# Kernel tuning notes

Measured on AMD Instinct MI355X. Metric: run time of the kernel, lower is better.

The kernel has to match this reference:

```python
import jax, jax.numpy as jnp
import numpy as np

B, H, W = 4, 192, 192
CIN, CB, CM = 64, 16, 256   # backbone out, bottleneck, mask channels
TOPK = 16
TEMP = 1.0
COLOR_NORM = 1.0
BN_EPS = 1e-5


def setup_inputs() -> dict:
    key = jax.random.key(0)
    k0, k1, k2, k3 = jax.random.split(key, 4)
    img = jax.random.uniform(k0, (B, 3, H, W), jnp.float32)
    base_feat = jax.random.normal(k1, (B, CIN, H, W), jnp.float32)
    w_bneck = jax.random.normal(k2, (CB, CIN), jnp.float32) * 0.05
    b_bneck = jnp.zeros((CB,), jnp.float32)
    bn_gamma = jnp.ones((CB,), jnp.float32)
    bn_beta = jnp.zeros((CB,), jnp.float32)
    w_mask = jax.random.normal(k3, (CM, CB), jnp.float32) * 0.05
    return dict(img=img, base_feat=base_feat, w_bneck=w_bneck, b_bneck=b_bneck,
                bn_gamma=bn_gamma, bn_beta=bn_beta, w_mask=w_mask, num_colors=256)


def reference(img, base_feat, w_bneck, b_bneck, bn_gamma, bn_beta, w_mask, num_colors):
    b, _, h, w = img.shape
    # bottleneck: 1x1 conv + BatchNorm (training batch stats) + ReLU
    x = jnp.einsum('bchw,oc->bohw', base_feat, w_bneck) + b_bneck[None, :, None, None]
    mean = x.mean(axis=(0, 2, 3))
    var = x.var(axis=(0, 2, 3))
    x = (x - mean[None, :, None, None]) * jax.lax.rsqrt(var + BN_EPS)[None, :, None, None]
    feat = jax.nn.relu(x * bn_gamma[None, :, None, None] + bn_beta[None, :, None, None])
    # color mask: 1x1 conv (no bias) -> [B, 256, H, W]
    m = jnp.einsum('bchw,oc->bohw', feat, w_mask)
    # fold 256 channels into num_colors groups and sum -> [B, K, H, W]
    m = m.reshape(b, -1, num_colors, h, w).sum(axis=1)
    k = min(TOPK, num_colors)
    # top-k over the color axis, softmax, scatter back into sparse mask
    mt = jnp.transpose(m, (0, 2, 3, 1))              # [B, H, W, K]
    vals, idx = jax.lax.top_k(mt, k)                 # [B, H, W, k]
    sm = jax.nn.softmax(vals / TEMP, axis=-1)
    m_sp = jnp.zeros_like(mt).at[
        jnp.arange(b)[:, None, None, None],
        jnp.arange(h)[None, :, None, None],
        jnp.arange(w)[None, None, :, None],
        idx].set(sm)
    m_sp = jnp.transpose(m_sp, (0, 3, 1, 2))         # [B, K, H, W]
    # weighted color palette: avoid the [B,3,K,H,W] intermediate via einsum
    num = jnp.einsum('bchw,bkhw->bck', img, m_sp)    # [B, 3, K]
    den = m_sp.sum(axis=(2, 3))[:, None, :] + 1e-8   # [B, 1, K]
    color_palette = num / den / COLOR_NORM           # [B, 3, K]
    transformed_img = jnp.einsum('bkhw,bck->bchw', m_sp, color_palette)
    return transformed_img, m_sp, color_palette[:, :, :, None, None]
```

## Files before the change

kernel.cpp:

```cpp
#include <hip/hip_runtime.h>

#define HW    36864
#define NB    4
#define NCH   256
#define CIN   64
#define CB    16
#define NPIX  (NB*HW)
#define DELTA 1e-4f

typedef short bf16x8 __attribute__((ext_vector_type(8)));
typedef float f32x4  __attribute__((ext_vector_type(4)));

struct FlagEntry {
  unsigned pix;
  unsigned char cnt, need, r0, r1;
  unsigned char ks[8];
};


__device__ __forceinline__ unsigned short bf16_rne(float x) {
  unsigned u = __float_as_uint(x);
  unsigned r = u + 0x7fffu + ((u >> 16) & 1u);
  return (unsigned short)(r >> 16);
}
__device__ __forceinline__ float bf16_tof(unsigned short h) {
  return __uint_as_float(((unsigned)h) << 16);
}


template<bool ASC>
__device__ __forceinline__ void bitonic16(float* v) {
  #pragma unroll
  for (int K = 2; K <= 16; K <<= 1) {
    #pragma unroll
    for (int J = K >> 1; J > 0; J >>= 1) {
      #pragma unroll
      for (int i = 0; i < 16; ++i) {
        int l = i ^ J;
        if (l > i) {
          bool up = (((i & K) == 0) == ASC);
          float a = v[i], b = v[l];
          float lo = fminf(a, b), hi = fmaxf(a, b);
          v[i] = up ? lo : hi;
          v[l] = up ? hi : lo;
        }
      }
    }
  }
}

__device__ __forceinline__ void bmerge16_desc(float* v) {
  #pragma unroll
  for (int J = 8; J > 0; J >>= 1) {
    #pragma unroll
    for (int i = 0; i < 16; ++i) {
      int l = i ^ J;
      if (l > i) {
        float a = v[i], b = v[l];
        float lo = fminf(a, b), hi = fmaxf(a, b);
        v[i] = hi; v[l] = lo;
      }
    }
  }
}


__global__ void k0_zero(unsigned* flagcnt) { *flagcnt = 0u; }


__global__ __launch_bounds__(256) void k1_conv(
    const float* __restrict__ bfeat, const float* __restrict__ wb,
    const float* __restrict__ bb, float* __restrict__ xout,
    double* __restrict__ part)
{
  __shared__ float wbT[CIN][CB];
  __shared__ double redS[4][CB];
  __shared__ double redQ[4][CB];
  const int t = threadIdx.x;
  for (int i = t; i < CIN*CB; i += 256) {
    int o = i >> 6, c = i & 63;
    wbT[c][o] = wb[i];
  }
  __syncthreads();

  const int blk = blockIdx.x;
  const int b = blk / 144, seg = blk % 144;
  const int p = seg * 256 + t;
  const float* bfb = bfeat + (size_t)b * CIN * HW;

  float acc[CB];
  #pragma unroll
  for (int o = 0; o < CB; ++o) acc[o] = bb[o];

  for (int c = 0; c < CIN; ++c) {
    float v = bfb[(size_t)c*HW + p];
    #pragma unroll
    for (int o4 = 0; o4 < 4; ++o4) {
      float4 w4 = *(const float4*)&wbT[c][o4*4];
      acc[o4*4+0] = fmaf(v, w4.x, acc[o4*4+0]);
      acc[o4*4+1] = fmaf(v, w4.y, acc[o4*4+1]);
      acc[o4*4+2] = fmaf(v, w4.z, acc[o4*4+2]);
      acc[o4*4+3] = fmaf(v, w4.w, acc[o4*4+3]);
    }
  }

  float* xb = xout + (size_t)b * CB * HW;
  #pragma unroll
  for (int o = 0; o < CB; ++o) xb[(size_t)o*HW + p] = acc[o];

  const int wv = t >> 6, lane = t & 63;
  #pragma unroll
  for (int o = 0; o < CB; ++o) {
    double a = (double)acc[o], q = a*a;
    for (int off = 32; off; off >>= 1) { a += __shfl_xor(a, off); q += __shfl_xor(q, off); }
    if (lane == 0) { redS[wv][o] = a; redQ[wv][o] = q; }
  }
  __syncthreads();
  if (t < CB) {
    double a = redS[0][t] + redS[1][t] + redS[2][t] + redS[3][t];
    part[(size_t)blk*32 + t] = a;
  } else if (t < 32) {
    int o = t - CB;
    double q = redQ[0][o] + redQ[1][o] + redQ[2][o] + redQ[3][o];
    part[(size_t)blk*32 + t] = q;
  }
}


__global__ __launch_bounds__(64) void k1b_stats(
    const double* __restrict__ part, const float* __restrict__ gam,
    const float* __restrict__ bet, double* __restrict__ st64, float* __restrict__ st32)
{
  __shared__ double sh[32];
  const int t = threadIdx.x;
  if (t < 32) {
    double a = 0.0;
    #pragma unroll 8
    for (int i = 0; i < 576; ++i) a += part[(size_t)i*32 + t];
    sh[t] = a;
  }
  __syncthreads();
  if (t < CB) {
    const double N = (double)NPIX;
    double mean = sh[t] / N;
    double var  = sh[16+t] / N - mean*mean;
    double rstd = 1.0 / sqrt(var + 1e-5);
    double scl = (double)gam[t] * rstd;
    double sft = (double)bet[t] - mean*scl;
    st64[t] = scl; st64[CB+t] = sft;
    st32[t] = (float)scl; st32[CB+t] = (float)sft;
  }
}


__global__ __launch_bounds__(256) void k1c_bfrag(
    const float* __restrict__ wm, short* __restrict__ bfrag)
{
  const int t = threadIdx.x;
  for (int e = t; e < 2048; e += 256) {
    const int v = e >> 10, ct = (e >> 6) & 15, l = e & 63;
    const int n = l & 15, g = l >> 4;
    const int col = ct*16 + n;
    short out[8];
    #pragma unroll
    for (int j = 0; j < 8; ++j) {
      const int k = g*8 + j;
      const int kk = k & 15;
      const bool hi_half = (k < 16);
      float w = wm[col*CB + kk];
      unsigned short hb = bf16_rne(w);
      float res = w - bf16_tof(hb);
      unsigned short lb = bf16_rne(res);
      bool use_hi = ((v == 0) == hi_half);
      out[j] = (short)(use_hi ? hb : lb);
    }
    bf16x8 pk;
    #pragma unroll
    for (int j = 0; j < 8; ++j) pk[j] = out[j];
    *(bf16x8*)&bfrag[(size_t)e * 8] = pk;
  }
}


__device__ __forceinline__ void k2_epilogue(int b, int p, int pxl,
    int selN, int nearN, int nselN,
    float* lcw, unsigned char* lidx, unsigned char* lnear,
    unsigned* cidx, float* cw, unsigned* flagcnt, FlagEntry* entries)
{
  int start = selN < 16 ? selN : 16;
  for (int j = start; j < 16; ++j) { lcw[pxl*16 + j] = 0.f; lidx[pxl*16 + j] = 0; }
  unsigned g = (unsigned)(b*HW + p);
  uint4 iv = *(uint4*)&lidx[pxl*16];
  ((uint4*)cidx)[g] = iv;
  float4* cwq = (float4*)cw;
  #pragma unroll
  for (int q = 0; q < 4; ++q) cwq[(size_t)g*4 + q] = *(float4*)&lcw[pxl*16 + q*4];
  bool flag = (nearN > 1) || (selN != 16);
  if (flag) {
    unsigned slot = atomicAdd(flagcnt, 1u);
    FlagEntry e;
    e.pix = g;
    int cnt = nearN < 8 ? nearN : 8;
    e.cnt = (unsigned char)cnt;
    int nsure = selN - nselN;
    int need = 16 - nsure;
    if (need < 0) need = 0;
    if (need > cnt) need = cnt;
    e.need = (unsigned char)need;
    e.r0 = (nearN > 8 || selN != 16) ? 1 : 0;
    e.r1 = 0;
    #pragma unroll
    for (int j = 0; j < 8; ++j) e.ks[j] = (j < cnt) ? lnear[pxl*8 + j] : 0;
    entries[slot] = e;
  }
}

#define MSTRIDE 260
#define PXB 32

__global__ __launch_bounds__(256, 4) void k2_main(
    const float* __restrict__ x, const short* __restrict__ bfrag,
    const float* __restrict__ st32, float* __restrict__ msp,
    unsigned* __restrict__ cidx, float* __restrict__ cw,
    unsigned* __restrict__ flagcnt, FlagEntry* __restrict__ entries)
{
  extern __shared__ char smem[];
  float* m_lds = (float*)smem;
  char* uni = smem + PXB*MSTRIDE*4;
  float* lcw = (float*)uni;
  unsigned char* lidx  = (unsigned char*)(uni + 2048);
  unsigned char* lnear = (unsigned char*)(uni + 2560);
  short* A_st = (short*)uni;

  const int t = threadIdx.x;
  const int blk = blockIdx.x;
  const int b = blk / 1152;
  const int p0 = (blk % 1152) * PXB;
  const float* xb = x + (size_t)b*CB*HW + p0;

  #pragma unroll
  for (int r = 0; r < 2; ++r) {
    int e = r*256 + t;
    int o = e >> 5, pl = e & 31;
    float vx = xb[(size_t)o*HW + pl];
    float f = fmaxf(0.f, fmaf(vx, st32[o], st32[CB+o]));
    unsigned short hb = bf16_rne(f);
    float res = f - bf16_tof(hb);
    unsigned short lb = bf16_rne(res);
    A_st[pl*40 + o]      = (short)hb;
    A_st[pl*40 + 16 + o] = (short)lb;
  }
  __syncthreads();

  const int w = t >> 6, l = t & 63;

  {
    const int rt = w & 1, ch = w >> 1;
    const int prow = rt*16 + (l & 15);
    const int k0 = (l >> 4) * 8;
    bf16x8 a = *(const bf16x8*)&A_st[prow*40 + k0];
    const int rowo = rt*16 + (l >> 4)*4;
    const int coln = l & 15;
    #pragma unroll
    for (int cc = 0; cc < 8; ++cc) {
      const int ct = ch*8 + cc;
      bf16x8 b1 = *(const bf16x8*)&bfrag[(size_t)(ct*64 + l)*8];
      bf16x8 b2 = *(const bf16x8*)&bfrag[(size_t)((16 + ct)*64 + l)*8];
      f32x4 acc = {0.f, 0.f, 0.f, 0.f};
      acc = __builtin_amdgcn_mfma_f32_16x16x32_bf16(a, b1, acc, 0, 0, 0);
      acc = __builtin_amdgcn_mfma_f32_16x16x32_bf16(a, b2, acc, 0, 0, 0);
      #pragma unroll
      for (int i = 0; i < 4; ++i)
        m_lds[(rowo + i)*MSTRIDE + ct*16 + coln] = acc[i];
    }
  }
  __syncthreads();

  const int p = t >> 3, q = t & 7;
  float mv[32];
  #pragma unroll
  for (int r = 0; r < 8; ++r) {
    const int c = (r + q) & 7;
    f32x4 v4 = *(const f32x4*)&m_lds[p*MSTRIDE + q*32 + c*4];
    mv[c*4+0] = v4[0]; mv[c*4+1] = v4[1]; mv[c*4+2] = v4[2]; mv[c*4+3] = v4[3];
  }

  float T[16], tmp[16];
  #pragma unroll
  for (int i = 0; i < 16; ++i) tmp[i] = mv[i];
  bitonic16<false>(tmp);
  #pragma unroll
  for (int i = 0; i < 16; ++i) T[i] = tmp[i];
  #pragma unroll
  for (int i = 0; i < 16; ++i) tmp[i] = mv[16 + i];
  bitonic16<true>(tmp);
  #pragma unroll
  for (int i = 0; i < 16; ++i) T[i] = fmaxf(T[i], tmp[i]);
  bmerge16_desc(T);
  #pragma unroll
  for (int mk = 1; mk <= 4; mk <<= 1) {
    float R[16];
    #pragma unroll
    for (int i = 0; i < 16; ++i) R[i] = fmaxf(T[i], __shfl_xor(T[15-i], mk));
    bmerge16_desc(R);
    #pragma unroll
    for (int i = 0; i < 16; ++i) T[i] = R[i];
  }
  const float tau = T[15], top = T[0];
  float Z = 0.f;
  #pragma unroll
  for (int i = 0; i < 16; ++i) Z += __expf(T[i] - top);
  const float iZ = 1.f / Z;

  int cs = 0, cn = 0, cns = 0;
  #pragma unroll
  for (int j = 0; j < 32; ++j) {
    float v = mv[j];
    bool s = (v >= tau);
    bool nr = (fabsf(v - tau) <= DELTA);
    cs += s ? 1 : 0; cn += nr ? 1 : 0; cns += (s && nr) ? 1 : 0;
  }
  const int lb_ = l & ~7;
  int offs = 0, offn = 0, selN = 0, nearN = 0, nselN = 0;
  #pragma unroll
  for (int j2 = 0; j2 < 8; ++j2) {
    int cv = __shfl(cs, lb_ + j2);
    int nv = __shfl(cn, lb_ + j2);
    int sv = __shfl(cns, lb_ + j2);
    selN += cv; nearN += nv; nselN += sv;
    if (j2 < q) { offs += cv; offn += nv; }
  }

  float* mspb = msp + (size_t)b*NCH*HW + p0;
  int isel = 0, inear = 0;
  #pragma unroll
  for (int j = 0; j < 32; ++j) {
    const int k = q*32 + j;
    float v = mv[j];
    bool s = (v >= tau);
    bool nr = (fabsf(v - tau) <= DELTA);
    float wv = s ? __expf(v - top) * iZ : 0.f;
    mspb[(size_t)k*HW + p] = wv;
    if (s) {
      int slot = offs + isel;
      if (slot < 16) { lcw[p*16 + slot] = wv; lidx[p*16 + slot] = (unsigned char)k; }
      ++isel;
    }
    if (nr) {
      int gs = offn + inear;
      if (gs < 8) lnear[p*8 + gs] = (unsigned char)k;
      ++inear;
    }
  }

  if (q == 0)
    k2_epilogue(b, p0 + p, p, selN, nearN, nselN, lcw, lidx, lnear,
                cidx, cw, flagcnt, entries);
}


__global__ __launch_bounds__(64) void k2b_fix(
    const float* __restrict__ bfeat, const float* __restrict__ wb,
    const float* __restrict__ bb, const float* __restrict__ wmg,
    const double* __restrict__ st64,
    const unsigned* __restrict__ flagcnt, const FlagEntry* __restrict__ entries,
    float* __restrict__ msp, unsigned* __restrict__ cidx, float* __restrict__ cw)
{
  __shared__ float wbT[CB][CIN];
  __shared__ float  wOrigL[16];
  __shared__ int    kOrigL[16];
  __shared__ float  wnL[8];
  __shared__ int    kL[8];
  __shared__ double tvL[16];
  __shared__ int    tiL[16];
  __shared__ float  wvL[16];

  const int lane = threadIdx.x;
  for (int i = lane; i < CB*CIN; i += 64) wbT[i >> 6][i & 63] = wb[i];
  __syncthreads();

  const unsigned n = *flagcnt;
  for (unsigned idx = blockIdx.x; idx < n; idx += gridDim.x) {
    FlagEntry e = entries[idx];
    const int b = (int)(e.pix / HW), p = (int)(e.pix % HW);

    const double v = (double)bfeat[(size_t)b*CIN*HW + (size_t)lane*HW + p];
    double ft[CB];
    #pragma unroll
    for (int o = 0; o < CB; ++o) {
      double s = v * (double)wbT[o][lane];
      #pragma unroll
      for (int off = 32; off; off >>= 1) s += __shfl_xor(s, off);
      s += (double)bb[o];
      ft[o] = fmax(0.0, s*st64[o] + st64[CB+o]);
    }

    float* mb = msp + (size_t)b*NCH*HW;
    unsigned char* cb_ = (unsigned char*)cidx + (size_t)e.pix*16;
    float* cwp = cw + (size_t)e.pix*16;

    if (e.r0) {
      double mm[4]; int kk4[4];
      #pragma unroll
      for (int u = 0; u < 4; ++u) {
        const int k = lane + 64*u; kk4[u] = k;
        const float* wr = wmg + k*CB;
        double a = 0.0;
        #pragma unroll
        for (int c = 0; c < CB; ++c) a = fma(ft[c], (double)wr[c], a);
        mm[u] = a;
      }
      for (int j = 0; j < 16; ++j) {
        double bm = mm[0]; int bk = kk4[0];
        #pragma unroll
        for (int u = 1; u < 4; ++u) {
          bool gt = (mm[u] > bm) || (mm[u] == bm && kk4[u] < bk);
          if (gt) { bm = mm[u]; bk = kk4[u]; }
        }
        #pragma unroll
        for (int off = 32; off; off >>= 1) {
          double om = __shfl_xor(bm, off);
          int ok = __shfl_xor(bk, off);
          bool gt = (om > bm) || (om == bm && ok < bk);
          if (gt) { bm = om; bk = ok; }
        }
        if (lane == 0) { tvL[j] = bm; tiL[j] = bk; }
        #pragma unroll
        for (int u = 0; u < 4; ++u) if (kk4[u] == bk) mm[u] = -1.0e300;
      }
      __syncthreads();
      const double top = tvL[0];
      double ej = (lane < 16) ? exp(tvL[lane] - top) : 0.0;
      double Z = ej;
      #pragma unroll
      for (int off = 32; off; off >>= 1) Z += __shfl_xor(Z, off);
      if (lane < 16) wvL[lane] = (float)(ej / Z);
      __syncthreads();
      int tiR[16]; float wvR[16];
      #pragma unroll
      for (int j = 0; j < 16; ++j) { tiR[j] = tiL[j]; wvR[j] = wvL[j]; }
      #pragma unroll
      for (int u = 0; u < 4; ++u) {
        const int k = lane + 64*u;
        float wv = 0.f;
        #pragma unroll
        for (int j = 0; j < 16; ++j) if (tiR[j] == k) wv = wvR[j];
        mb[(size_t)k*HW + p] = wv;
      }
      if (lane == 0) {
        unsigned used = 0; int on = 0;
        for (int it = 0; it < 16; ++it) {
          int bk = 1 << 20;
          #pragma unroll
          for (int j = 0; j < 16; ++j)
            if (!((used >> j) & 1u) && tiR[j] < bk) bk = tiR[j];
          if (bk >= (1 << 20)) break;
          float bw = 0.f;
          #pragma unroll
          for (int j = 0; j < 16; ++j)
            if (tiR[j] == bk) { bw = wvR[j]; used |= (1u << j); }
          if (bw != 0.f && on < 16) { cb_[on] = (unsigned char)bk; cwp[on] = bw; ++on; }
        }
        for (int j = on; j < 16; ++j) { cb_[j] = 0; cwp[j] = 0.f; }
      }
      __syncthreads();
      continue;
    }

    const int cnt = (e.cnt > 8) ? 8 : (int)e.cnt;
    int need = (int)e.need; if (need > cnt) need = cnt;

    if (lane < 16) { wOrigL[lane] = cwp[lane]; kOrigL[lane] = (int)cb_[lane]; }
    __syncthreads();

    const int myk = (lane < cnt) ? (int)e.ks[lane] : 0x7fffffff;
    double mj = 0.0;
    if (lane < cnt) {
      const float* wr = wmg + myk*CB;
      #pragma unroll
      for (int c = 0; c < CB; ++c) mj = fma(ft[c], (double)wr[c], mj);
    }
    float woldj = 0.f;
    if (lane < cnt) {
      #pragma unroll
      for (int q = 0; q < 16; ++q) {
        if (kOrigL[q] == myk && wOrigL[q] > 0.f) woldj = wOrigL[q];
      }
    }
    int rankj = 0;
    #pragma unroll
    for (int j2 = 0; j2 < 8; ++j2) {
      double m2 = __shfl(mj, j2);
      int k2v = __shfl(myk, j2);
      if (lane < cnt && j2 < cnt && j2 != lane) {
        bool gt = (m2 > mj) || (m2 == mj && k2v < myk);
        rankj += gt ? 1 : 0;
      }
    }
    float w2[8];
    #pragma unroll
    for (int j2 = 0; j2 < 8; ++j2) w2[j2] = __shfl(woldj, j2);
    int nw = 0;
    #pragma unroll
    for (int j2 = 0; j2 < 8; ++j2) if (j2 < cnt && w2[j2] > 0.f) ++nw;
    float wnj = 0.f;
    if (lane < cnt && rankj < need && rankj < nw) {
      #pragma unroll
      for (int cand = 0; cand < 8; ++cand) {
        if (cand < cnt && w2[cand] > 0.f) {
          float xv = w2[cand];
          int cgt = 0, cge = 0;
          #pragma unroll
          for (int j2 = 0; j2 < 8; ++j2)
            if (j2 < cnt && w2[j2] > 0.f) { cgt += (w2[j2] > xv); cge += (w2[j2] >= xv); }
          if (cgt <= rankj && rankj < cge) wnj = xv;
        }
      }
    }
    if (lane < cnt) mb[(size_t)myk*HW + p] = wnj;
    if (lane < 8)  { wnL[lane] = wnj; kL[lane] = myk; }
    __syncthreads();

    if (lane == 0) {
      int on = 0, ii = 0, jj = 0;
      while (ii < 16 || jj < cnt) {
        if (ii < 16 && wOrigL[ii] <= 0.f) { ++ii; continue; }
        int ko = (ii < 16) ? kOrigL[ii] : (1 << 20);
        int kj = (jj < cnt) ? kL[jj] : (1 << 20);
        if (ko >= (1 << 20) && kj >= (1 << 20)) break;
        if (ko < kj) {
          if (on < 16) { cb_[on] = (unsigned char)ko; cwp[on] = wOrigL[ii]; ++on; }
          ++ii;
        } else if (kj < ko) {
          if (wnL[jj] > 0.f && on < 16) { cb_[on] = (unsigned char)kj; cwp[on] = wnL[jj]; ++on; }
          ++jj;
        } else {
          if (wnL[jj] > 0.f && on < 16) { cb_[on] = (unsigned char)kj; cwp[on] = wnL[jj]; ++on; }
          ++ii; ++jj;
        }
      }
      for (int j = on; j < 16; ++j) { cb_[j] = 0; cwp[j] = 0.f; }
    }
    __syncthreads();
  }
}


__global__ __launch_bounds__(256) void k3_accum(
    const uint4* __restrict__ cidx, const float4* __restrict__ cw4,
    const float* __restrict__ img, float* __restrict__ part)
{
  __shared__ float acc[1024];
  const int t = threadIdx.x, blk = blockIdx.x;
  for (int i = t; i < 1024; i += 256) acc[i] = 0.f;
  __syncthreads();
  const int b = blk / 144;
  const int p = (blk % 144) * 256 + t;
  const float* imb = img + (size_t)b*3*HW;
  const int g = b*HW + p;
  uint4 iv = cidx[g];
  unsigned ivq[4] = {iv.x, iv.y, iv.z, iv.w};
  float r = imb[p], g_ = imb[HW + p], bl = imb[2*HW + p];
  #pragma unroll
  for (int q = 0; q < 4; ++q) {
    float4 wv = cw4[(size_t)g*4 + q];
    float wvv[4] = {wv.x, wv.y, wv.z, wv.w};
    #pragma unroll
    for (int u = 0; u < 4; ++u) {
      int k = (int)((ivq[q] >> (8*u)) & 255u);
      float wgt = wvv[u];
      atomicAdd(&acc[k],       wgt * r);
      atomicAdd(&acc[256 + k], wgt * g_);
      atomicAdd(&acc[512 + k], wgt * bl);
      atomicAdd(&acc[768 + k], wgt);
    }
  }
  __syncthreads();
  for (int i = t; i < 1024; i += 256) part[(size_t)blk*1024 + i] = acc[i];
}


__global__ __launch_bounds__(256) void k4_pal(
    const float* __restrict__ part, float* __restrict__ out_pal)
{
  __shared__ float acc[1024];
  const int b = blockIdx.x, t = threadIdx.x;
  for (int s = t; s < 1024; s += 256) {
    float a = 0.f;
    for (int i = 0; i < 144; ++i) a += part[(size_t)(b*144 + i)*1024 + s];
    acc[s] = a;
  }
  __syncthreads();
  for (int s = t; s < 768; s += 256) {
    int k = s & 255;
    float den = acc[768 + k] + 1e-8f;
    out_pal[(size_t)b*768 + s] = acc[s] / den;
  }
}


__global__ __launch_bounds__(256) void k5_img(
    const uint4* __restrict__ cidx, const float4* __restrict__ cw4,
    const float* __restrict__ pal, float* __restrict__ outimg)
{
  __shared__ float lp[768];
  const int t = threadIdx.x, blk = blockIdx.x;
  const int b = blk / 144;
  for (int i = t; i < 768; i += 256) lp[i] = pal[(size_t)b*768 + i];
  __syncthreads();
  const int p = (blk % 144) * 256 + t;
  const int g = b*HW + p;
  uint4 iv = cidx[g];
  unsigned ivq[4] = {iv.x, iv.y, iv.z, iv.w};
  float r = 0.f, g_ = 0.f, bl = 0.f;
  #pragma unroll
  for (int q = 0; q < 4; ++q) {
    float4 wv = cw4[(size_t)g*4 + q];
    float wvv[4] = {wv.x, wv.y, wv.z, wv.w};
    #pragma unroll
    for (int u = 0; u < 4; ++u) {
      int k = (int)((ivq[q] >> (8*u)) & 255u);
      float wgt = wvv[u];
      r  = fmaf(wgt, lp[k],       r);
      g_ = fmaf(wgt, lp[256 + k], g_);
      bl = fmaf(wgt, lp[512 + k], bl);
    }
  }
  float* ob = outimg + (size_t)b*3*HW;
  ob[p] = r; ob[HW + p] = g_; ob[2*HW + p] = bl;
}


extern "C" void kernel_launch(void* const* d_in, const int* in_sizes, int n_in,
                              void* d_out, int out_size, void* d_ws, size_t ws_size,
                              hipStream_t stream)
{
  const float* img   = (const float*)d_in[0];
  const float* bfeat = (const float*)d_in[1];
  const float* wb    = (const float*)d_in[2];
  const float* bb    = (const float*)d_in[3];
  const float* gam   = (const float*)d_in[4];
  const float* bet   = (const float*)d_in[5];
  const float* wm    = (const float*)d_in[6];

  float* out_img = (float*)d_out;
  float* out_msp = (float*)d_out + 442368;
  float* out_pal = (float*)d_out + 38191104;

  char* w = (char*)d_ws;
  float*     ws_x       = (float*)(w);
  double*    ws_part    = (double*)(w + 9437184);
  double*    ws_st64    = (double*)(w + 9584640);
  float*     ws_st32    = (float*)(w + 9584896);
  unsigned*  ws_flagcnt = (unsigned*)(w + 9585152);
  FlagEntry* ws_entries = (FlagEntry*)(w + 9585408);
  unsigned*  ws_cidx    = (unsigned*)(w + 11944704);
  float*     ws_cw      = (float*)(w + 14304000);
  float*     ws_nd      = ws_x;
  short*     ws_bfrag   = (short*)(w + 23741184);

  k0_zero<<<dim3(1), dim3(1), 0, stream>>>(ws_flagcnt);
  k1_conv<<<dim3(576), dim3(256), 0, stream>>>(bfeat, wb, bb, ws_x, ws_part);
  k1b_stats<<<dim3(1), dim3(64), 0, stream>>>(ws_part, gam, bet, ws_st64, ws_st32);
  k1c_bfrag<<<dim3(1), dim3(256), 0, stream>>>(wm, ws_bfrag);
  k2_main<<<dim3(4608), dim3(256), 36096, stream>>>(ws_x, ws_bfrag, ws_st32, out_msp,
                                                    ws_cidx, ws_cw, ws_flagcnt, ws_entries);
  k2b_fix<<<dim3(4096), dim3(64), 0, stream>>>(bfeat, wb, bb, wm, ws_st64,
                                               ws_flagcnt, ws_entries, out_msp, ws_cidx, ws_cw);
  k3_accum<<<dim3(576), dim3(256), 0, stream>>>((const uint4*)ws_cidx, (const float4*)ws_cw,
                                                img, ws_nd);
  k4_pal<<<dim3(4), dim3(256), 0, stream>>>(ws_nd, out_pal);
  k5_img<<<dim3(576), dim3(256), 0, stream>>>((const uint4*)ws_cidx, (const float4*)ws_cw,
                                              out_pal, out_img);
}
```

Before: 314.2 us.

## Split fused MFMA+top-k kernel into separate matmul and per-pixel selection kernels

The fused k2_main kernel is split in two. k2a_mfma computes the 256-channel mask via MFMA and writes raw logits to the output buffer. k2s_sel then rereads them with one thread per pixel, runs a streaming bitonic top-16, and rewrites the sparse softmax weights. This removes the cross-lane shuffle merges and the 8-lanes-per-pixel layout, but adds a full extra read and write of the roughly 150 MB mask tensor through global memory.

```diff
diff --git a/kernel.cpp b/kernel.cpp
--- a/kernel.cpp
+++ b/kernel.cpp
@@ -178,6 +178,73 @@
     #pragma unroll
     for (int j = 0; j < 8; ++j) pk[j] = out[j];
     *(bf16x8*)&bfrag[(size_t)e * 8] = pk;
+  }
+}
+
+
+#define MSTRIDE 261
+#define PXB 32
+
+__global__ __launch_bounds__(256, 4) void k2a_mfma(
+    const float* __restrict__ x, const short* __restrict__ bfrag,
+    const float* __restrict__ st32, float* __restrict__ msp)
+{
+  extern __shared__ char smem[];
+  float* m_lds = (float*)smem;
+  short* A_st = (short*)(smem + PXB*MSTRIDE*4);
+
+  const int t = threadIdx.x;
+  const int blk = blockIdx.x;
+  const int b = blk / 1152;
+  const int p0 = (blk % 1152) * PXB;
+  const float* xb = x + (size_t)b*CB*HW + p0;
+
+  #pragma unroll
+  for (int r = 0; r < 2; ++r) {
+    int e = r*256 + t;
+    int o = e >> 5, pl = e & 31;
+    float vx = xb[(size_t)o*HW + pl];
+    float f = fmaxf(0.f, fmaf(vx, st32[o], st32[CB+o]));
+    unsigned short hb = bf16_rne(f);
+    float res = f - bf16_tof(hb);
+    unsigned short lb = bf16_rne(res);
+    A_st[pl*40 + o]      = (short)hb;
+    A_st[pl*40 + 16 + o] = (short)lb;
+  }
+  __syncthreads();
+
+  const int w = t >> 6, l = t & 63;
+
+  {
+    const int rt = w & 1, ch = w >> 1;
+    const int prow = rt*16 + (l & 15);
+    const int k0 = (l >> 4) * 8;
+    bf16x8 a = *(const bf16x8*)&A_st[prow*40 + k0];
+    const int rowo = rt*16 + (l >> 4)*4;
+    const int coln = l & 15;
+    #pragma unroll
+    for (int cc = 0; cc < 8; ++cc) {
+      const int ct = ch*8 + cc;
+      bf16x8 b1 = *(const bf16x8*)&bfrag[(size_t)(ct*64 + l)*8];
+      bf16x8 b2 = *(const bf16x8*)&bfrag[(size_t)((16 + ct)*64 + l)*8];
+      f32x4 acc = {0.f, 0.f, 0.f, 0.f};
+      acc = __builtin_amdgcn_mfma_f32_16x16x32_bf16(a, b1, acc, 0, 0, 0);
+      acc = __builtin_amdgcn_mfma_f32_16x16x32_bf16(a, b2, acc, 0, 0, 0);
+      #pragma unroll
+      for (int i = 0; i < 4; ++i)
+        m_lds[(rowo + i)*MSTRIDE + ct*16 + coln] = acc[i];
+    }
+  }
+  __syncthreads();
+
+  {
+    const int pp = t & 31, kq = t >> 5;
+    float* mspb = msp + (size_t)b*NCH*HW + p0 + pp;
+    #pragma unroll
+    for (int j = 0; j < 32; ++j) {
+      const int k = kq*32 + j;
+      mspb[(size_t)k*HW] = m_lds[pp*MSTRIDE + k];
+    }
   }
 }
 
@@ -215,147 +282,63 @@
   }
 }
 
-#define MSTRIDE 260
-#define PXB 32
-
-__global__ __launch_bounds__(256, 4) void k2_main(
-    const float* __restrict__ x, const short* __restrict__ bfrag,
-    const float* __restrict__ st32, float* __restrict__ msp,
+__global__ __launch_bounds__(256) void k2s_sel(
+    float* __restrict__ msp,
     unsigned* __restrict__ cidx, float* __restrict__ cw,
     unsigned* __restrict__ flagcnt, FlagEntry* __restrict__ entries)
 {
-  extern __shared__ char smem[];
-  float* m_lds = (float*)smem;
-  char* uni = smem + PXB*MSTRIDE*4;
-  float* lcw = (float*)uni;
-  unsigned char* lidx  = (unsigned char*)(uni + 2048);
-  unsigned char* lnear = (unsigned char*)(uni + 2560);
-  short* A_st = (short*)uni;
-
+  __shared__ float lcw[256*16];
+  __shared__ __align__(16) unsigned char lidx[256*16];
+  __shared__ unsigned char lnear[256*8];
   const int t = threadIdx.x;
   const int blk = blockIdx.x;
-  const int b = blk / 1152;
-  const int p0 = (blk % 1152) * PXB;
-  const float* xb = x + (size_t)b*CB*HW + p0;
-
-  #pragma unroll
-  for (int r = 0; r < 2; ++r) {
-    int e = r*256 + t;
-    int o = e >> 5, pl = e & 31;
-    float vx = xb[(size_t)o*HW + pl];
-    float f = fmaxf(0.f, fmaf(vx, st32[o], st32[CB+o]));
-    unsigned short hb = bf16_rne(f);
-    float res = f - bf16_tof(hb);
-    unsigned short lb = bf16_rne(res);
-    A_st[pl*40 + o]      = (short)hb;
-    A_st[pl*40 + 16 + o] = (short)lb;
-  }
-  __syncthreads();
-
-  const int w = t >> 6, l = t & 63;
-
+  const int b = blk / 144;
+  const int p = (blk % 144) * 256 + t;
+  float* mspb = msp + (size_t)b*NCH*HW;
+
+  float T[16];
   {
-    const int rt = w & 1, ch = w >> 1;
-    const int prow = rt*16 + (l & 15);
-    const int k0 = (l >> 4) * 8;
-    bf16x8 a = *(const bf16x8*)&A_st[prow*40 + k0];
-    const int rowo = rt*16 + (l >> 4)*4;
-    const int coln = l & 15;
-    #pragma unroll
-    for (int cc = 0; cc < 8; ++cc) {
-      const int ct = ch*8 + cc;
-      bf16x8 b1 = *(const bf16x8*)&bfrag[(size_t)(ct*64 + l)*8];
-      bf16x8 b2 = *(const bf16x8*)&bfrag[(size_t)((16 + ct)*64 + l)*8];
-      f32x4 acc = {0.f, 0.f, 0.f, 0.f};
-      acc = __builtin_amdgcn_mfma_f32_16x16x32_bf16(a, b1, acc, 0, 0, 0);
-      acc = __builtin_amdgcn_mfma_f32_16x16x32_bf16(a, b2, acc, 0, 0, 0);
-      #pragma unroll
-      for (int i = 0; i < 4; ++i)
-        m_lds[(rowo + i)*MSTRIDE + ct*16 + coln] = acc[i];
-    }
-  }
-  __syncthreads();
-
-  const int p = t >> 3, q = t & 7;
-  float mv[32];
-  #pragma unroll
-  for (int r = 0; r < 8; ++r) {
-    const int c = (r + q) & 7;
-    f32x4 v4 = *(const f32x4*)&m_lds[p*MSTRIDE + q*32 + c*4];
-    mv[c*4+0] = v4[0]; mv[c*4+1] = v4[1]; mv[c*4+2] = v4[2]; mv[c*4+3] = v4[3];
-  }
-
-  float T[16], tmp[16];
-  #pragma unroll
-  for (int i = 0; i < 16; ++i) tmp[i] = mv[i];
-  bitonic16<false>(tmp);
-  #pragma unroll
-  for (int i = 0; i < 16; ++i) T[i] = tmp[i];
-  #pragma unroll
-  for (int i = 0; i < 16; ++i) tmp[i] = mv[16 + i];
-  bitonic16<true>(tmp);
-  #pragma unroll
-  for (int i = 0; i < 16; ++i) T[i] = fmaxf(T[i], tmp[i]);
-  bmerge16_desc(T);
-  #pragma unroll
-  for (int mk = 1; mk <= 4; mk <<= 1) {
-    float R[16];
-    #pragma unroll
-    for (int i = 0; i < 16; ++i) R[i] = fmaxf(T[i], __shfl_xor(T[15-i], mk));
-    bmerge16_desc(R);
-    #pragma unroll
-    for (int i = 0; i < 16; ++i) T[i] = R[i];
+    float m[16];
+    #pragma unroll
+    for (int kk = 0; kk < 16; ++kk) m[kk] = mspb[(size_t)kk*HW + p];
+    bitonic16<false>(m);
+    #pragma unroll
+    for (int i = 0; i < 16; ++i) T[i] = m[i];
+  }
+  for (int ch = 1; ch < 16; ++ch) {
+    float m[16];
+    #pragma unroll
+    for (int kk = 0; kk < 16; ++kk) m[kk] = mspb[(size_t)(ch*16 + kk)*HW + p];
+    bitonic16<true>(m);
+    #pragma unroll
+    for (int i = 0; i < 16; ++i) T[i] = fmaxf(T[i], m[i]);
+    bmerge16_desc(T);
   }
   const float tau = T[15], top = T[0];
   float Z = 0.f;
   #pragma unroll
-  for (int i = 0; i < 16; ++i) Z += __expf(T[i] - top);
-  const float iZ = 1.f / Z;
-
-  int cs = 0, cn = 0, cns = 0;
-  #pragma unroll
-  for (int j = 0; j < 32; ++j) {
-    float v = mv[j];
-    bool s = (v >= tau);
-    bool nr = (fabsf(v - tau) <= DELTA);
-    cs += s ? 1 : 0; cn += nr ? 1 : 0; cns += (s && nr) ? 1 : 0;
-  }
-  const int lb_ = l & ~7;
-  int offs = 0, offn = 0, selN = 0, nearN = 0, nselN = 0;
-  #pragma unroll
-  for (int j2 = 0; j2 < 8; ++j2) {
-    int cv = __shfl(cs, lb_ + j2);
-    int nv = __shfl(cn, lb_ + j2);
-    int sv = __shfl(cns, lb_ + j2);
-    selN += cv; nearN += nv; nselN += sv;
-    if (j2 < q) { offs += cv; offn += nv; }
-  }
-
-  float* mspb = msp + (size_t)b*NCH*HW + p0;
-  int isel = 0, inear = 0;
-  #pragma unroll
-  for (int j = 0; j < 32; ++j) {
-    const int k = q*32 + j;
-    float v = mv[j];
-    bool s = (v >= tau);
-    bool nr = (fabsf(v - tau) <= DELTA);
-    float wv = s ? __expf(v - top) * iZ : 0.f;
-    mspb[(size_t)k*HW + p] = wv;
-    if (s) {
-      int slot = offs + isel;
-      if (slot < 16) { lcw[p*16 + slot] = wv; lidx[p*16 + slot] = (unsigned char)k; }
-      ++isel;
-    }
-    if (nr) {
-      int gs = offn + inear;
-      if (gs < 8) lnear[p*8 + gs] = (unsigned char)k;
-      ++inear;
-    }
-  }
-
-  if (q == 0)
-    k2_epilogue(b, p0 + p, p, selN, nearN, nselN, lcw, lidx, lnear,
-                cidx, cw, flagcnt, entries);
+  for (int i = 0; i < 16; ++i) Z += __expf(T[i]-top);
+  const float iZ = 1.f/Z;
+
+  int sel = 0, nearc = 0, nsel = 0;
+  for (int ch = 0; ch < 16; ++ch) {
+    float m[16];
+    #pragma unroll
+    for (int kk = 0; kk < 16; ++kk) m[kk] = mspb[(size_t)(ch*16 + kk)*HW + p];
+    #pragma unroll
+    for (int kk = 0; kk < 16; ++kk) {
+      const int k = ch*16 + kk;
+      const float v = m[kk];
+      const bool s = (v >= tau);
+      const bool nr = (fabsf(v - tau) <= DELTA);
+      float wv = 0.f;
+      if (s) wv = __expf(v - top) * iZ;
+      mspb[(size_t)k*HW + p] = wv;
+      if (s) { if (sel < 16) { lcw[t*16 + sel] = wv; lidx[t*16 + sel] = (unsigned char)k; } ++sel; if (nr) ++nsel; }
+      if (nr) { if (nearc < 8) lnear[t*8 + nearc] = (unsigned char)k; ++nearc; }
+    }
+  }
+  k2_epilogue(b, p, t, sel, nearc, nsel, lcw, lidx, lnear, cidx, cw, flagcnt, entries);
 }
 
 
@@ -663,8 +646,9 @@
   k1_conv<<<dim3(576), dim3(256), 0, stream>>>(bfeat, wb, bb, ws_x, ws_part);
   k1b_stats<<<dim3(1), dim3(64), 0, stream>>>(ws_part, gam, bet, ws_st64, ws_st32);
   k1c_bfrag<<<dim3(1), dim3(256), 0, stream>>>(wm, ws_bfrag);
-  k2_main<<<dim3(4608), dim3(256), 36096, stream>>>(ws_x, ws_bfrag, ws_st32, out_msp,
-                                                    ws_cidx, ws_cw, ws_flagcnt, ws_entries);
+  k2a_mfma<<<dim3(4608), dim3(256), 35968, stream>>>(ws_x, ws_bfrag, ws_st32, out_msp);
+  k2s_sel<<<dim3(576), dim3(256), 0, stream>>>(out_msp, ws_cidx, ws_cw,
+                                               ws_flagcnt, ws_entries);
   k2b_fix<<<dim3(4096), dim3(64), 0, stream>>>(bfeat, wb, bb, wm, ws_st64,
                                                ws_flagcnt, ws_entries, out_msp, ws_cidx, ws_cw);
   k3_accum<<<dim3(576), dim3(256), 0, stream>>>((const uint4*)ws_cidx, (const float4*)ws_cw,
```

Result: no change. 319.3 us (+1.6%).
